# Performance work log

Hardware: AMD Instinct MI355X
Metric: run time of the kernel (lower is better)

Reference implementation:

```python
import jax, jax.numpy as jnp
import numpy as np

B = 4096          # number of graphs / embeddings
EMB = 768         # smiles embedding dim
HID = 64          # hidden_dim
NODE_DIM = 64     # GCN input feature dim (hard-coded in CombinedSparseModel)
N_NODES = 262144
N_EDGES = 1048576
N_HEADS = 4
TOPK = 5


def _lin(key, fi, fo):
    s = 1.0 / np.sqrt(fi)
    kw, kb = jax.random.split(key)
    w = jax.random.uniform(kw, (fi, fo), minval=-s, maxval=s, dtype=jnp.float32)
    b = jax.random.uniform(kb, (fo,), minval=-s, maxval=s, dtype=jnp.float32)
    return w, b


def setup_inputs() -> dict:
    key = jax.random.key(0)
    ks = jax.random.split(key, 20)
    inp = {
        'smiles_embedding': jax.random.normal(ks[0], (B, 1, EMB), dtype=jnp.float32),
        'node_x': jax.random.normal(ks[1], (N_NODES, NODE_DIM), dtype=jnp.float32),
        'edge_src': jax.random.randint(ks[2], (N_EDGES,), 0, N_NODES),
        'edge_dst': jax.random.randint(ks[3], (N_EDGES,), 0, N_NODES),
        'batch_vec': jnp.sort(jax.random.randint(ks[4], (N_NODES,), 0, B)),
    }
    layers = [('emb_w1', 'emb_b1', EMB, 1024), ('emb_w2', 'emb_b2', 1024, HID),
              ('g1_w', 'g1_b', NODE_DIM, NODE_DIM), ('g2_w', 'g2_b', NODE_DIM, 2 * NODE_DIM),
              ('gfc_w', 'gfc_b', 2 * NODE_DIM, HID),
              ('q_w', 'q_b', 2 * HID, 2 * HID), ('k_w', 'k_b', 2 * HID, 2 * HID),
              ('v_w', 'v_b', 2 * HID, 2 * HID), ('o_w', 'o_b', 2 * HID, 2 * HID),
              ('f1_w', 'f1_b', 2 * HID, HID), ('ff_w', 'ff_b', HID, 1)]
    for i, (wn, bn, fi, fo) in enumerate(layers):
        w, b = _lin(ks[5 + i], fi, fo)
        inp[wn] = w
        inp[bn] = b
    return inp


def gcn_conv(x, w, b, src, dst, n_nodes):
    # PyG GCNConv: h = D^-1/2 (A+I) D^-1/2 (x W) + b
    h = x @ w
    loops = jnp.arange(n_nodes)
    s = jnp.concatenate([src, loops])
    d = jnp.concatenate([dst, loops])
    deg = jax.ops.segment_sum(jnp.ones_like(d, dtype=h.dtype), d, num_segments=n_nodes)
    dinv = jax.lax.rsqrt(deg)            # deg >= 1 due to self loops
    norm = dinv[s] * dinv[d]             # [E+N]
    msg = h[s] * norm[:, None]
    return jax.ops.segment_sum(msg, d, num_segments=n_nodes) + b


def sparse_attention(x, q_w, q_b, k_w, k_b, v_w, v_b, o_w, o_b):
    bsz, S, E = x.shape
    hd = E // N_HEADS
    k = min(TOPK, S)

    def split(t):
        return t.reshape(bsz, S, N_HEADS, hd).transpose(0, 2, 1, 3)  # [b,h,s,d]

    Q = split(x @ q_w + q_b)
    K = split(x @ k_w + k_b)
    V = split(x @ v_w + v_b)
    scores = jnp.einsum('bhqd,bhkd->bhqk', Q, K) / jnp.asarray(np.sqrt(hd), jnp.float32)
    _, idx = jax.lax.top_k(scores, k)
    # scatter 1s at top-k key positions (indices within a row are distinct)
    mask = jax.nn.one_hot(idx, S, dtype=scores.dtype).sum(axis=-2)  # [b,h,q,S]
    attn = jax.nn.softmax(scores * mask, axis=-1)
    out = jnp.einsum('bhqk,bhkd->bhqd', attn, V)
    out = out.transpose(0, 2, 1, 3).reshape(bsz, S, E)
    return out @ o_w + o_b


def reference(smiles_embedding, node_x, edge_src, edge_dst, batch_vec, emb_w1, emb_b1, emb_w2, emb_b2, g1_w, g1_b, g2_w, g2_b, gfc_w, gfc_b, q_w, q_b, k_w, k_b, v_w, v_b, o_w, o_b, f1_w, f1_b, ff_w, ff_b):
    # EmbeddingDNN (dropout = identity in eval mode)
    e = jax.nn.relu(smiles_embedding @ emb_w1 + emb_b1) @ emb_w2 + emb_b2  # [B,1,HID]
    # GCN branch
    h = jax.nn.relu(gcn_conv(node_x, g1_w, g1_b, edge_src, edge_dst, N_NODES))
    h = gcn_conv(h, g2_w, g2_b, edge_src, edge_dst, N_NODES)               # [N,2*NODE_DIM]
    cnt = jax.ops.segment_sum(jnp.ones((N_NODES,), h.dtype), batch_vec, num_segments=B)
    pooled = jax.ops.segment_sum(h, batch_vec, num_segments=B) / jnp.maximum(cnt, 1.0)[:, None]
    g = pooled @ gfc_w + gfc_b                                             # [B,HID]
    combined = jnp.concatenate([e, g[:, None, :]], axis=2)                 # [B,1,2*HID]
    a = sparse_attention(combined, q_w, q_b, k_w, k_b, v_w, v_b, o_w, o_b)[:, 0]
    z = a @ f1_w + f1_b
    return z @ ff_w + ff_b                                                 # [B,1]
```

## Files before the change

### kernel.cpp

```cpp
#include <hip/hip_runtime.h>

#define NNODES 262144
#define NEDGES 1048576
#define NB     4096

typedef __attribute__((ext_vector_type(8))) short short8v;
typedef __attribute__((ext_vector_type(4))) float f32x4;

__device__ __forceinline__ unsigned short f2bf(float f) {
    unsigned int u = __float_as_uint(f);
    u += 0x7FFFu + ((u >> 16) & 1u);
    return (unsigned short)(u >> 16);
}
__device__ __forceinline__ float bf2f(unsigned short h) {
    return __uint_as_float((unsigned int)h << 16);
}

__global__ __launch_bounds__(256) void emb_mfma(
    const float* __restrict__ A, const float* __restrict__ B,
    const float* __restrict__ bias, const float* __restrict__ v1,
    float* __restrict__ epart)
{
    __shared__ __align__(16) unsigned short Asb[64][80];
    __shared__ __align__(16) unsigned short Btb[64][80];
    __shared__ float red[64][16];
    const int tid = threadIdx.x;
    const int w = tid >> 6, lane = tid & 63;
    const int m0 = blockIdx.x * 64, n0 = blockIdx.y * 64;

    f32x4 acc[4] = {{0.f,0.f,0.f,0.f},{0.f,0.f,0.f,0.f},
                    {0.f,0.f,0.f,0.f},{0.f,0.f,0.f,0.f}};

    const int ar = tid >> 2, ak4 = (tid & 3) * 4;
    const int bk = tid >> 2, bc4 = (tid & 3) * 4;

    for (int k0 = 0; k0 < 768; k0 += 64) {
        __syncthreads();
        {
            const float* src = A + (size_t)(m0 + ar) * 768 + k0 + ak4;
#pragma unroll
            for (int rep = 0; rep < 4; ++rep) {
                float4 v = *(const float4*)(src + rep * 16);
                unsigned long long pk =
                      (unsigned long long)f2bf(v.x)
                    | ((unsigned long long)f2bf(v.y) << 16)
                    | ((unsigned long long)f2bf(v.z) << 32)
                    | ((unsigned long long)f2bf(v.w) << 48);
                *(unsigned long long*)&Asb[ar][ak4 + rep * 16] = pk;
            }
        }
        {
            const float* src = B + (size_t)(k0 + bk) * 1024 + n0 + bc4;
#pragma unroll
            for (int rep = 0; rep < 4; ++rep) {
                float4 v = *(const float4*)(src + rep * 16);
                Btb[bc4 + rep * 16 + 0][bk] = f2bf(v.x);
                Btb[bc4 + rep * 16 + 1][bk] = f2bf(v.y);
                Btb[bc4 + rep * 16 + 2][bk] = f2bf(v.z);
                Btb[bc4 + rep * 16 + 3][bk] = f2bf(v.w);
            }
        }
        __syncthreads();
#pragma unroll
        for (int ks = 0; ks < 2; ++ks) {
            short8v af = *(const short8v*)&Asb[w * 16 + (lane & 15)][ks * 32 + 8 * (lane >> 4)];
#pragma unroll
            for (int ct = 0; ct < 4; ++ct) {
                short8v bf = *(const short8v*)&Btb[ct * 16 + (lane & 15)][ks * 32 + 8 * (lane >> 4)];
                acc[ct] = __builtin_amdgcn_mfma_f32_16x16x32_bf16(af, bf, acc[ct], 0, 0, 0);
            }
        }
    }

    float p[4] = {0.f, 0.f, 0.f, 0.f};
#pragma unroll
    for (int ct = 0; ct < 4; ++ct) {
        const int col = n0 + ct * 16 + (lane & 15);
        const float bcv = bias[col], vcv = v1[col];
#pragma unroll
        for (int i = 0; i < 4; ++i)
            p[i] += fmaxf(acc[ct][i] + bcv, 0.f) * vcv;
    }
#pragma unroll
    for (int i = 0; i < 4; ++i)
        red[w * 16 + 4 * (lane >> 4) + i][lane & 15] = p[i];
    __syncthreads();
    if (tid < 64) {
        float s = 0.f;
#pragma unroll
        for (int c = 0; c < 16; ++c) s += red[tid][c];
        epart[(size_t)(m0 + tid) * 16 + blockIdx.y] = s;
    }
}

__global__ __launch_bounds__(256) void gemm_y(
    const float* __restrict__ A, const float* __restrict__ B,
    const float* __restrict__ dinv, unsigned short* __restrict__ Ys)
{
    __shared__ float As[16][64];
    __shared__ float Bs[16][64];
    const int tid = threadIdx.x;
    const int tx = tid & 15, ty = tid >> 4;
    const int m0 = blockIdx.x * 64;

    float acc[4][4] = {};
    const int ar = tid >> 2, aseg = tid & 3;
    const int bk = tid >> 4, bseg = tid & 15;
    const float* Aptr = A + (size_t)(m0 + ar) * 64 + aseg * 4;
    const float* Bptr = B + (size_t)bk * 64 + bseg * 4;

    for (int k0 = 0; k0 < 64; k0 += 16) {
        float4 av = *(const float4*)(Aptr + k0);
        float4 bv = *(const float4*)(Bptr + (size_t)k0 * 64);
        __syncthreads();
        As[aseg * 4 + 0][ar] = av.x;
        As[aseg * 4 + 1][ar] = av.y;
        As[aseg * 4 + 2][ar] = av.z;
        As[aseg * 4 + 3][ar] = av.w;
        *(float4*)&Bs[bk][bseg * 4] = bv;
        __syncthreads();
#pragma unroll
        for (int k = 0; k < 16; ++k) {
            float4 a4 = *(const float4*)&As[k][ty * 4];
            float4 b4 = *(const float4*)&Bs[k][tx * 4];
            float aa[4] = {a4.x, a4.y, a4.z, a4.w};
            float bb[4] = {b4.x, b4.y, b4.z, b4.w};
#pragma unroll
            for (int i = 0; i < 4; ++i)
#pragma unroll
                for (int j = 0; j < 4; ++j)
                    acc[i][j] += aa[i] * bb[j];
        }
    }

#pragma unroll
    for (int i = 0; i < 4; ++i) {
        const int row = m0 + ty * 4 + i;
        const float dv = dinv[row];
        unsigned short h4[4];
#pragma unroll
        for (int j = 0; j < 4; ++j) h4[j] = f2bf(acc[i][j] * dv);
        *(unsigned long long*)&Ys[(size_t)row * 64 + tx * 4] =
              (unsigned long long)h4[0]
            | ((unsigned long long)h4[1] << 16)
            | ((unsigned long long)h4[2] << 32)
            | ((unsigned long long)h4[3] << 48);
    }
}

__global__ void count_deg(const int* __restrict__ dst, int* __restrict__ deg)
{
    int i = blockIdx.x * 256 + threadIdx.x;
    if (i < NEDGES) atomicAdd(&deg[dst[i]], 1);
}

__global__ void make_dinv(const int* __restrict__ deg, float* __restrict__ dinv)
{
    int i = blockIdx.x * 256 + threadIdx.x;
    if (i < NNODES) dinv[i] = rsqrtf((float)(deg[i] + 1));
}

__global__ __launch_bounds__(1024) void scan_block(
    const int* __restrict__ in, int* __restrict__ out, int* __restrict__ bsums)
{
    __shared__ int tmp[1024];
    const int tid = threadIdx.x;
    const int gid = blockIdx.x * 1024 + tid;
    int v = in[gid];
    tmp[tid] = v;
    __syncthreads();
    for (int off = 1; off < 1024; off <<= 1) {
        int t = (tid >= off) ? tmp[tid - off] : 0;
        __syncthreads();
        tmp[tid] += t;
        __syncthreads();
    }
    out[gid] = tmp[tid] - v;
    if (tid == 1023) bsums[blockIdx.x] = tmp[tid];
}

__global__ __launch_bounds__(256) void scan_top(int* __restrict__ bsums)
{
    __shared__ int tmp[256];
    const int tid = threadIdx.x;
    int v = bsums[tid];
    tmp[tid] = v;
    __syncthreads();
    for (int off = 1; off < 256; off <<= 1) {
        int t = (tid >= off) ? tmp[tid - off] : 0;
        __syncthreads();
        tmp[tid] += t;
        __syncthreads();
    }
    bsums[tid] = tmp[tid] - v;
}

__global__ void scan_add(int* __restrict__ out, const int* __restrict__ bsums)
{
    int gid = blockIdx.x * 256 + threadIdx.x;
    out[gid] += bsums[gid >> 10];
}

__global__ void scatter_edges(const int* __restrict__ src, const int* __restrict__ dst,
                              int* __restrict__ cur, int* __restrict__ csr)
{
    int i = blockIdx.x * 256 + threadIdx.x;
    if (i < NEDGES) {
        int d = dst[i];
        int pos = atomicAdd(&cur[d], 1);
        csr[pos] = src[i];
    }
}

__global__ __launch_bounds__(256) void agg_dot(
    const unsigned short* __restrict__ Ys, const int* __restrict__ offs,
    const int* __restrict__ csr, const float* __restrict__ dinv,
    const float* __restrict__ g1_b, const float* __restrict__ v2,
    float* __restrict__ td)
{
    const int q = (blockIdx.x * 256 + threadIdx.x) >> 6;
    const int lane = threadIdx.x & 63;
    const int n0 = q * 4;
    if (n0 >= NNODES) return;

    const int o0 = offs[n0];
    const int o1 = offs[n0 + 1];
    const int o2 = offs[n0 + 2];
    const int o3 = offs[n0 + 3];
    const int o4 = (n0 + 4 < NNODES) ? offs[n0 + 4] : NEDGES;

    float a0 = bf2f(Ys[(size_t)(n0 + 0) * 64 + lane]);
    float a1 = bf2f(Ys[(size_t)(n0 + 1) * 64 + lane]);
    float a2 = bf2f(Ys[(size_t)(n0 + 2) * 64 + lane]);
    float a3 = bf2f(Ys[(size_t)(n0 + 3) * 64 + lane]);

    int e = o0;
    for (; e + 8 <= o4; e += 8) {
        int s[8];
#pragma unroll
        for (int u = 0; u < 8; ++u) s[u] = csr[e + u];
        float hv[8];
#pragma unroll
        for (int u = 0; u < 8; ++u) hv[u] = bf2f(Ys[(size_t)s[u] * 64 + lane]);
#pragma unroll
        for (int u = 0; u < 8; ++u) {
            const int ei = e + u;
            if      (ei < o1) a0 += hv[u];
            else if (ei < o2) a1 += hv[u];
            else if (ei < o3) a2 += hv[u];
            else              a3 += hv[u];
        }
    }
    for (; e < o4; ++e) {
        const float c = bf2f(Ys[(size_t)csr[e] * 64 + lane]);
        if      (e < o1) a0 += c;
        else if (e < o2) a1 += c;
        else if (e < o3) a2 += c;
        else             a3 += c;
    }

    const float bb = g1_b[lane], vv = v2[lane];
    float t0 = fmaxf(a0 * dinv[n0 + 0] + bb, 0.f) * vv;
    float t1 = fmaxf(a1 * dinv[n0 + 1] + bb, 0.f) * vv;
    float t2 = fmaxf(a2 * dinv[n0 + 2] + bb, 0.f) * vv;
    float t3 = fmaxf(a3 * dinv[n0 + 3] + bb, 0.f) * vv;
#pragma unroll
    for (int off = 32; off; off >>= 1) {
        t0 += __shfl_down(t0, off, 64);
        t1 += __shfl_down(t1, off, 64);
        t2 += __shfl_down(t2, off, 64);
        t3 += __shfl_down(t3, off, 64);
    }
    if (lane == 0) {
        td[n0 + 0] = t0 * dinv[n0 + 0];
        td[n0 + 1] = t1 * dinv[n0 + 1];
        td[n0 + 2] = t2 * dinv[n0 + 2];
        td[n0 + 3] = t3 * dinv[n0 + 3];
    }
}

__global__ void agg_scalar(
    const float* __restrict__ td, const int* __restrict__ offs,
    const int* __restrict__ csr, const float* __restrict__ dinv,
    float* __restrict__ z)
{
    int i = blockIdx.x * 256 + threadIdx.x;
    if (i >= NNODES) return;
    float s = td[i];
    const int e0 = offs[i];
    const int e1 = (i + 1 < NNODES) ? offs[i + 1] : NEDGES;
    for (int e = e0; e < e1; ++e) s += td[csr[e]];
    z[i] = s * dinv[i];
}

__global__ __launch_bounds__(256) void pool_dot(
    const float* __restrict__ z, const int* __restrict__ start,
    const float* __restrict__ cntinv, float* __restrict__ gpart)
{
    const int g = (blockIdx.x * 256 + threadIdx.x) >> 6;
    const int lane = threadIdx.x & 63;
    if (g >= NB) return;
    const int s0 = start[g], s1 = start[g + 1];
    float a = 0.f;
    for (int i = s0 + lane; i < s1; i += 64) a += z[i];
#pragma unroll
    for (int off = 32; off; off >>= 1) a += __shfl_down(a, off, 64);
    if (lane == 0) gpart[g] = a * cntinv[g];
}

__global__ void graph_starts(const int* __restrict__ bv, int* __restrict__ start)
{
    int g = blockIdx.x * 256 + threadIdx.x;
    if (g > NB) return;
    if (g == NB) { start[g] = NNODES; return; }
    int lo = 0, hi = NNODES;
    while (lo < hi) {
        int mid = (lo + hi) >> 1;
        if (bv[mid] < g) lo = mid + 1; else hi = mid;
    }
    start[g] = lo;
}

__global__ void make_cntinv(const int* __restrict__ start, float* __restrict__ cntinv)
{
    int g = blockIdx.x * 256 + threadIdx.x;
    if (g < NB) cntinv[g] = 1.0f / fmaxf((float)(start[g + 1] - start[g]), 1.0f);
}

__global__ __launch_bounds__(256) void precompute(
    const float* __restrict__ emb_w2, const float* __restrict__ emb_b2,
    const float* __restrict__ g2_w, const float* __restrict__ g2_b,
    const float* __restrict__ gfc_w, const float* __restrict__ gfc_b,
    const float* __restrict__ v_b,
    const float* __restrict__ o_w, const float* __restrict__ o_b,
    const float* __restrict__ f1_w, const float* __restrict__ f1_b,
    const float* __restrict__ ff_w, const float* __restrict__ ff_b,
    const float* __restrict__ v_w, float* __restrict__ pre)
{
    const int tid = threadIdx.x;
    float* p1 = pre;
    float* p2 = pre + 128;
    float* wf = pre + 256;
    float* q1 = pre + 384;
    float* v2 = pre + 512;
    float* v1 = pre + 576;

    if (tid < 128) {
        float s = 0.f;
        for (int k = 0; k < 64; ++k) s += f1_w[tid * 64 + k] * ff_w[k];
        p1[tid] = s;
    }
    __syncthreads();
    if (tid < 128) {
        float s = 0.f;
        for (int k = 0; k < 128; ++k) s += o_w[tid * 128 + k] * p1[k];
        p2[tid] = s;
    }
    __syncthreads();
    if (tid < 128) {
        float s = 0.f;
        for (int k = 0; k < 128; ++k) s += v_w[tid * 128 + k] * p2[k];
        wf[tid] = s;
    }
    __syncthreads();
    if (tid < 128) {
        float s = 0.f;
        for (int k = 0; k < 64; ++k) s += gfc_w[tid * 64 + k] * wf[64 + k];
        q1[tid] = s;
    }
    __syncthreads();
    if (tid < 64) {
        float s = 0.f;
        for (int k = 0; k < 128; ++k) s += g2_w[tid * 128 + k] * q1[k];
        v2[tid] = s;
    }
    for (int r = 0; r < 4; ++r) {
        int j = tid + 256 * r;
        float s = 0.f;
        for (int k = 0; k < 64; ++k) s += emb_w2[j * 64 + k] * wf[k];
        v1[j] = s;
    }
    if (tid == 0) {
        float c = ff_b[0];
        for (int k = 0; k < 64; ++k)  c += f1_b[k] * ff_w[k];
        for (int i = 0; i < 128; ++i) c += o_b[i] * p1[i] + v_b[i] * p2[i];
        for (int k = 0; k < 64; ++k)  c += emb_b2[k] * wf[k];
        for (int i = 0; i < 128; ++i) c += g2_b[i] * q1[i];
        for (int k = 0; k < 64; ++k)  c += gfc_b[k] * wf[64 + k];
        pre[1600] = c;
    }
}

__global__ void final_combine(
    const float* __restrict__ epart, const float* __restrict__ gpart,
    const float* __restrict__ pre, float* __restrict__ out)
{
    int b = blockIdx.x * 256 + threadIdx.x;
    if (b >= NB) return;
    float s = pre[1600] + gpart[b];
    const float* ep = &epart[(size_t)b * 16];
#pragma unroll
    for (int c = 0; c < 16; ++c) s += ep[c];
    out[b] = s;
}

extern "C" void kernel_launch(void* const* d_in, const int* in_sizes, int n_in,
                              void* d_out, int out_size, void* d_ws, size_t ws_size,
                              hipStream_t stream)
{
    const float* smiles = (const float*)d_in[0];
    const float* node_x = (const float*)d_in[1];
    const int*   esrc   = (const int*)d_in[2];
    const int*   edst   = (const int*)d_in[3];
    const int*   bvec   = (const int*)d_in[4];
    const float* emb_w1 = (const float*)d_in[5];
    const float* emb_b1 = (const float*)d_in[6];
    const float* emb_w2 = (const float*)d_in[7];
    const float* emb_b2 = (const float*)d_in[8];
    const float* g1_w   = (const float*)d_in[9];
    const float* g1_b   = (const float*)d_in[10];
    const float* g2_w   = (const float*)d_in[11];
    const float* g2_b   = (const float*)d_in[12];
    const float* gfc_w  = (const float*)d_in[13];
    const float* gfc_b  = (const float*)d_in[14];
    const float* v_w    = (const float*)d_in[19];
    const float* v_b    = (const float*)d_in[20];
    const float* o_w    = (const float*)d_in[21];
    const float* o_b    = (const float*)d_in[22];
    const float* f1_w   = (const float*)d_in[23];
    const float* f1_b   = (const float*)d_in[24];
    const float* ff_w   = (const float*)d_in[25];
    const float* ff_b   = (const float*)d_in[26];
    float* out = (float*)d_out;

    char* ws = (char*)d_ws;
    size_t off = 0;
    auto alloc = [&](size_t b) -> void* {
        void* p = ws + off;
        off += (b + 255) & ~(size_t)255;
        return p;
    };
    unsigned short* Ys = (unsigned short*)alloc((size_t)NNODES * 64 * 2);
    int*   deg    = (int*)alloc((size_t)NNODES * 4);
    int*   offs   = (int*)alloc((size_t)NNODES * 4);
    int*   cur    = (int*)alloc((size_t)NNODES * 4);
    float* dinv   = (float*)alloc((size_t)NNODES * 4);
    int*   csr    = (int*)alloc((size_t)NEDGES * 4);
    int*   startg = (int*)alloc((size_t)(NB + 1) * 4);
    int*   bsums  = (int*)alloc(256 * 4);
    float* cntinv = (float*)alloc((size_t)NB * 4);
    float* epart  = (float*)alloc((size_t)NB * 16 * 4);
    float* td     = (float*)alloc((size_t)NNODES * 4);
    float* zbuf   = (float*)alloc((size_t)NNODES * 4);
    float* gpart  = (float*)alloc((size_t)NB * 4);
    float* pre    = (float*)alloc(2048 * 4);

    hipMemsetAsync(deg, 0, (size_t)NNODES * 4, stream);
    count_deg<<<NEDGES / 256, 256, 0, stream>>>(edst, deg);
    make_dinv<<<NNODES / 256, 256, 0, stream>>>(deg, dinv);
    scan_block<<<NNODES / 1024, 1024, 0, stream>>>(deg, offs, bsums);
    scan_top<<<1, 256, 0, stream>>>(bsums);
    scan_add<<<NNODES / 256, 256, 0, stream>>>(offs, bsums);
    hipMemcpyAsync(cur, offs, (size_t)NNODES * 4, hipMemcpyDeviceToDevice, stream);
    scatter_edges<<<NEDGES / 256, 256, 0, stream>>>(esrc, edst, cur, csr);
    graph_starts<<<(NB + 256) / 256, 256, 0, stream>>>(bvec, startg);
    make_cntinv<<<NB / 256, 256, 0, stream>>>(startg, cntinv);

    precompute<<<1, 256, 0, stream>>>(emb_w2, emb_b2, g2_w, g2_b, gfc_w, gfc_b,
                                      v_b, o_w, o_b, f1_w, f1_b, ff_w, ff_b,
                                      v_w, pre);

    emb_mfma<<<dim3(NB / 64, 16), 256, 0, stream>>>(smiles, emb_w1, emb_b1,
                                                    pre + 576, epart);

    gemm_y<<<NNODES / 64, 256, 0, stream>>>(node_x, g1_w, dinv, Ys);
    agg_dot<<<NNODES / 16, 256, 0, stream>>>(Ys, offs, csr, dinv,
                                             g1_b, pre + 512, td);
    agg_scalar<<<NNODES / 256, 256, 0, stream>>>(td, offs, csr, dinv, zbuf);
    pool_dot<<<NB / 4, 256, 0, stream>>>(zbuf, startg, cntinv, gpart);

    final_combine<<<NB / 256, 256, 0, stream>>>(epart, gpart, pre, out);
}
```

Baseline: 436.1 us.

## Build CSR via two-pass bucket partition with shared-memory atomics

Replaces global-atomic degree counting and the random-scatter CSR build with a radix-style bucket partition. Edges are first partitioned into 512 destination buckets using per-block histograms and a scan. Each bucket is then handled by one block that counts degrees and scatters into CSR using shared-memory atomics. This is meant to cut contended global atomics and random global writes, at the cost of an 8-byte pairs buffer and several extra kernel launches.

```diff
diff --git a/kernel.cpp b/kernel.cpp
--- a/kernel.cpp
+++ b/kernel.cpp
@@ -3,6 +3,10 @@
 #define NNODES 262144
 #define NEDGES 1048576
 #define NB     4096
+#define NBUCK  512
+#define BSHIFT 9
+#define NBLK_A 256
+#define CHUNK  4096
 
 typedef __attribute__((ext_vector_type(8))) short short8v;
 typedef __attribute__((ext_vector_type(4))) float f32x4;
@@ -148,10 +152,73 @@
     }
 }
 
-__global__ void count_deg(const int* __restrict__ dst, int* __restrict__ deg)
-{
-    int i = blockIdx.x * 256 + threadIdx.x;
-    if (i < NEDGES) atomicAdd(&deg[dst[i]], 1);
+__global__ __launch_bounds__(256) void bucket_hist(
+    const int* __restrict__ dst, int* __restrict__ bcnt)
+{
+    __shared__ int hist[NBUCK];
+    const int tid = threadIdx.x, blk = blockIdx.x;
+    for (int i = tid; i < NBUCK; i += 256) hist[i] = 0;
+    __syncthreads();
+    const int e0 = blk * CHUNK;
+    for (int i = tid; i < CHUNK; i += 256)
+        atomicAdd(&hist[dst[e0 + i] >> BSHIFT], 1);
+    __syncthreads();
+    for (int i = tid; i < NBUCK; i += 256)
+        bcnt[i * NBLK_A + blk] = hist[i];
+}
+
+__global__ __launch_bounds__(256) void bucket_part(
+    const int* __restrict__ src, const int* __restrict__ dst,
+    const int* __restrict__ bpos, unsigned long long* __restrict__ pairs)
+{
+    __shared__ int cur[NBUCK];
+    const int tid = threadIdx.x, blk = blockIdx.x;
+    for (int i = tid; i < NBUCK; i += 256)
+        cur[i] = bpos[i * NBLK_A + blk];
+    __syncthreads();
+    const int e0 = blk * CHUNK;
+    for (int i = tid; i < CHUNK; i += 256) {
+        const int d = dst[e0 + i], s = src[e0 + i];
+        const int pos = atomicAdd(&cur[d >> BSHIFT], 1);
+        pairs[pos] = ((unsigned long long)(unsigned int)d << 32) | (unsigned int)s;
+    }
+}
+
+__global__ __launch_bounds__(256) void bucket_deg(
+    const unsigned long long* __restrict__ pairs, const int* __restrict__ bpos,
+    int* __restrict__ deg)
+{
+    __shared__ int dl[512];
+    const int tid = threadIdx.x, b = blockIdx.x;
+    dl[tid] = 0; dl[tid + 256] = 0;
+    __syncthreads();
+    const int s0 = bpos[b * NBLK_A];
+    const int s1 = (b + 1 < NBUCK) ? bpos[(b + 1) * NBLK_A] : NEDGES;
+    const int base = b << BSHIFT;
+    for (int e = s0 + tid; e < s1; e += 256)
+        atomicAdd(&dl[(int)(pairs[e] >> 32) - base], 1);
+    __syncthreads();
+    deg[base + tid] = dl[tid];
+    deg[base + tid + 256] = dl[tid + 256];
+}
+
+__global__ __launch_bounds__(256) void bucket_scatter(
+    const unsigned long long* __restrict__ pairs, const int* __restrict__ bpos,
+    const int* __restrict__ offs, int* __restrict__ csr)
+{
+    __shared__ int cl[512];
+    const int tid = threadIdx.x, b = blockIdx.x;
+    const int base = b << BSHIFT;
+    cl[tid] = offs[base + tid];
+    cl[tid + 256] = offs[base + tid + 256];
+    __syncthreads();
+    const int s0 = bpos[b * NBLK_A];
+    const int s1 = (b + 1 < NBUCK) ? bpos[(b + 1) * NBLK_A] : NEDGES;
+    for (int e = s0 + tid; e < s1; e += 256) {
+        const unsigned long long p = pairs[e];
+        const int pos = atomicAdd(&cl[(int)(p >> 32) - base], 1);
+        csr[pos] = (int)(p & 0xFFFFFFFFull);
+    }
 }
 
 __global__ void make_dinv(const int* __restrict__ deg, float* __restrict__ dinv)
@@ -179,11 +246,11 @@
     if (tid == 1023) bsums[blockIdx.x] = tmp[tid];
 }
 
-__global__ __launch_bounds__(256) void scan_top(int* __restrict__ bsums)
+__global__ __launch_bounds__(256) void scan_top(int* __restrict__ bsums, int n)
 {
     __shared__ int tmp[256];
     const int tid = threadIdx.x;
-    int v = bsums[tid];
+    int v = (tid < n) ? bsums[tid] : 0;
     tmp[tid] = v;
     __syncthreads();
     for (int off = 1; off < 256; off <<= 1) {
@@ -192,24 +259,13 @@
         tmp[tid] += t;
         __syncthreads();
     }
-    bsums[tid] = tmp[tid] - v;
+    if (tid < n) bsums[tid] = tmp[tid] - v;
 }
 
 __global__ void scan_add(int* __restrict__ out, const int* __restrict__ bsums)
 {
     int gid = blockIdx.x * 256 + threadIdx.x;
     out[gid] += bsums[gid >> 10];
-}
-
-__global__ void scatter_edges(const int* __restrict__ src, const int* __restrict__ dst,
-                              int* __restrict__ cur, int* __restrict__ csr)
-{
-    int i = blockIdx.x * 256 + threadIdx.x;
-    if (i < NEDGES) {
-        int d = dst[i];
-        int pos = atomicAdd(&cur[d], 1);
-        csr[pos] = src[i];
-    }
 }
 
 __global__ __launch_bounds__(256) void agg_dot(
@@ -441,9 +497,11 @@
         return p;
     };
     unsigned short* Ys = (unsigned short*)alloc((size_t)NNODES * 64 * 2);
+    unsigned long long* pairs = (unsigned long long*)alloc((size_t)NEDGES * 8);
+    int*   bcnt   = (int*)alloc((size_t)NBUCK * NBLK_A * 4);
+    int*   bsumsA = (int*)alloc(256 * 4);
     int*   deg    = (int*)alloc((size_t)NNODES * 4);
     int*   offs   = (int*)alloc((size_t)NNODES * 4);
-    int*   cur    = (int*)alloc((size_t)NNODES * 4);
     float* dinv   = (float*)alloc((size_t)NNODES * 4);
     int*   csr    = (int*)alloc((size_t)NEDGES * 4);
     int*   startg = (int*)alloc((size_t)(NB + 1) * 4);
@@ -455,14 +513,18 @@
     float* gpart  = (float*)alloc((size_t)NB * 4);
     float* pre    = (float*)alloc(2048 * 4);
 
-    hipMemsetAsync(deg, 0, (size_t)NNODES * 4, stream);
-    count_deg<<<NEDGES / 256, 256, 0, stream>>>(edst, deg);
+    bucket_hist<<<NBLK_A, 256, 0, stream>>>(edst, bcnt);
+    scan_block<<<(NBUCK * NBLK_A) / 1024, 1024, 0, stream>>>(bcnt, bcnt, bsumsA);
+    scan_top<<<1, 256, 0, stream>>>(bsumsA, (NBUCK * NBLK_A) / 1024);
+    scan_add<<<(NBUCK * NBLK_A) / 256, 256, 0, stream>>>(bcnt, bsumsA);
+    bucket_part<<<NBLK_A, 256, 0, stream>>>(esrc, edst, bcnt, pairs);
+    bucket_deg<<<NBUCK, 256, 0, stream>>>(pairs, bcnt, deg);
     make_dinv<<<NNODES / 256, 256, 0, stream>>>(deg, dinv);
     scan_block<<<NNODES / 1024, 1024, 0, stream>>>(deg, offs, bsums);
-    scan_top<<<1, 256, 0, stream>>>(bsums);
+    scan_top<<<1, 256, 0, stream>>>(bsums, NNODES / 1024);
     scan_add<<<NNODES / 256, 256, 0, stream>>>(offs, bsums);
-    hipMemcpyAsync(cur, offs, (size_t)NNODES * 4, hipMemcpyDeviceToDevice, stream);
-    scatter_edges<<<NEDGES / 256, 256, 0, stream>>>(esrc, edst, cur, csr);
+    bucket_scatter<<<NBUCK, 256, 0, stream>>>(pairs, bcnt, offs, csr);
+
     graph_starts<<<(NB + 256) / 256, 256, 0, stream>>>(bvec, startg);
     make_cntinv<<<NB / 256, 256, 0, stream>>>(startg, cntinv);
 
```

Result: faster. 364.8 us (-16.3%).
